# Kernel optimization log

Hardware: AMD Instinct MI355X
Metric: run time of the kernel (lower is better)

## Reference

```python
import jax, jax.numpy as jnp
import numpy as np

H = 16        # num_heads
LN_EPS = 1e-6

def _ln(x, w, b):
    mu = x.mean(-1, keepdims=True)
    var = ((x - mu) ** 2).mean(-1, keepdims=True)
    return (x - mu) * jax.lax.rsqrt(var + LN_EPS) * w + b

def setup_inputs():
    key = jax.random.key(0)
    ks = jax.random.split(key, 6)
    B, L, S, D = 2, 8192, 512, 1024
    std = 0.02
    return {
        "q_in": jax.random.normal(ks[0], (B, L, D), jnp.float32),
        "kv_in": jax.random.normal(ks[1], (B, S, D), jnp.float32),
        "qn_w": jnp.ones((D,), jnp.float32),
        "qn_b": jnp.zeros((D,), jnp.float32),
        "kvn_w": jnp.ones((D,), jnp.float32),
        "kvn_b": jnp.zeros((D,), jnp.float32),
        "Wq": jax.random.normal(ks[2], (D, D), jnp.float32) * std,
        "Wk": jax.random.normal(ks[3], (D, D), jnp.float32) * std,
        "Wv": jax.random.normal(ks[4], (D, D), jnp.float32) * std,
        "Wo": jax.random.normal(ks[5], (D, D), jnp.float32) * std,
        "bo": jnp.zeros((D,), jnp.float32),
        "gate": jnp.ones((1,), jnp.float32),
    }

def reference(q_in, kv_in, qn_w, qn_b, kvn_w, kvn_b, Wq, Wk, Wv, Wo, bo, gate):
    b, l, hid = q_in.shape
    s = kv_in.shape[1]
    d = hid // H
    scale = d ** -0.5
    q_x = _ln(q_in, qn_w, qn_b)
    kv_x = _ln(kv_in, kvn_w, kvn_b)
    # torch Linear: y = x @ W.T  (weights stored [out, in])
    q = (q_x @ Wq.T).reshape(b, l, H, d).transpose(0, 2, 1, 3)   # [b,H,l,d]
    k = (kv_x @ Wk.T).reshape(b, s, H, d).transpose(0, 2, 1, 3)  # [b,H,s,d]
    v = (kv_x @ Wv.T).reshape(b, s, H, d).transpose(0, 2, 1, 3)  # [b,H,s,d]
    logits = jnp.einsum('bhld,bhsd->bhls', q, k) * scale
    attn = jax.nn.softmax(logits, axis=-1)                       # [b,H,l,s]
    # no-grad diagnostics
    attn_d = jax.lax.stop_gradient(attn).astype(jnp.float32)
    ent_per_head = -(attn_d * jnp.log(attn_d + 1e-9)).sum(-1).mean(axis=(0, 2))  # [H]
    mean_entropy = ent_per_head.mean()
    head_entropy_std = ent_per_head.std()  # population std (unbiased=False)
    top_k = min(4, s)
    top_mass = jax.lax.top_k(attn_d, top_k)[0].sum(-1).mean()
    out = jnp.einsum('bhls,bhsd->bhld', attn, v)
    out = out.transpose(0, 2, 1, 3).reshape(b, l, hid)
    out = (out @ Wo.T + bo) * gate  # dropout=0 -> identity; gate broadcasts
    return (out, mean_entropy, head_entropy_std, top_mass, gate[0])
```

## Files before the change

kernel.cpp:

```cpp
#include <hip/hip_runtime.h>
#include <stdint.h>
#include <stddef.h>


typedef __attribute__((ext_vector_type(8))) short bf16x8;
typedef __attribute__((ext_vector_type(4))) float f32x4;

#define MFMA(a, b, c) __builtin_amdgcn_mfma_f32_16x16x32_bf16((a), (b), (c), 0, 0, 0)
#define MED3(a, b, c) __builtin_amdgcn_fmed3f((a), (b), (c))

__device__ __forceinline__ float bf2f(unsigned short u) {
  union { unsigned int ui; float f; } cv; cv.ui = ((unsigned int)u) << 16; return cv.f;
}
__device__ __forceinline__ unsigned short f2bf(float f) {
  union { float f; unsigned int ui; } cv; cv.f = f;
  unsigned int u = cv.ui;
  u = u + 0x7fffu + ((u >> 16) & 1u);
  return (unsigned short)(u >> 16);
}
__device__ __forceinline__ unsigned int pk2(float a, float b) {
  union { float f; unsigned int u; } ua, ub; ua.f = a; ub.f = b;
  return __builtin_amdgcn_perm(ub.u, ua.u, 0x07060302u);
}
__device__ __forceinline__ bool is_fp32(const unsigned int* probe) {
  return probe[0] == 0x3F800000u;
}
__device__ __forceinline__ void gl2lds(const unsigned short* g, unsigned short* l) {
  __builtin_amdgcn_global_load_lds(
      (const __attribute__((address_space(1))) void*)(uintptr_t)g,
      (__attribute__((address_space(3))) void*)(unsigned int)(uintptr_t)l,
      16, 0, 0);
}

__device__ __forceinline__ size_t qf_addr(int qg, int d) {
  int b = qg >> 13, q = qg & 8191, h = d >> 6, dd = d & 63;
  int lane = (q & 15) | (((dd >> 3) & 3) << 4);
  return ((((size_t)(b * 16 + h) * 512 + (q >> 4)) * 2 + (dd >> 5)) * 64 + lane) * 8 + (dd & 7);
}
__device__ __forceinline__ size_t kf_addr(int r, int d) {
  int b = r >> 9, s = r & 511, h = d >> 6, dd = d & 63;
  int lane = (s & 15) | (((dd >> 3) & 3) << 4);
  return ((((size_t)(b * 16 + h) * 32 + (s >> 4)) * 2 + (dd >> 5)) * 64 + lane) * 8 + (dd & 7);
}
__device__ __forceinline__ size_t vf_addr(int r, int d) {
  int b = r >> 9, s = r & 511, h = d >> 6, dd = d & 63;
  int lane = (dd & 15) | (((s >> 3) & 3) << 4);
  return ((((size_t)(b * 16 + h) * 16 + (s >> 5)) * 4 + (dd >> 4)) * 64 + lane) * 8 + (s & 7);
}

__device__ __forceinline__ void ln_row_impl(
    bool f32, const void* __restrict__ xv, const void* __restrict__ wv,
    const void* __restrict__ bv, unsigned short* __restrict__ y,
    int row, int tid, float* rs, float* rs2)
{
  float v0, v1, v2, v3, w0, w1, w2, w3, b0, b1, b2, b3;
  if (f32) {
    float4 xr = *(const float4*)((const float*)xv + (size_t)row * 1024 + tid * 4);
    v0 = xr.x; v1 = xr.y; v2 = xr.z; v3 = xr.w;
    float4 wr = *(const float4*)((const float*)wv + tid * 4);
    w0 = wr.x; w1 = wr.y; w2 = wr.z; w3 = wr.w;
    float4 br = *(const float4*)((const float*)bv + tid * 4);
    b0 = br.x; b1 = br.y; b2 = br.z; b3 = br.w;
  } else {
    ushort4 xr = *(const ushort4*)((const unsigned short*)xv + (size_t)row * 1024 + tid * 4);
    v0 = bf2f(xr.x); v1 = bf2f(xr.y); v2 = bf2f(xr.z); v3 = bf2f(xr.w);
    ushort4 wr = *(const ushort4*)((const unsigned short*)wv + tid * 4);
    w0 = bf2f(wr.x); w1 = bf2f(wr.y); w2 = bf2f(wr.z); w3 = bf2f(wr.w);
    ushort4 br = *(const ushort4*)((const unsigned short*)bv + tid * 4);
    b0 = bf2f(br.x); b1 = bf2f(br.y); b2 = bf2f(br.z); b3 = bf2f(br.w);
  }
  float s  = v0 + v1 + v2 + v3;
  float s2 = v0*v0 + v1*v1 + v2*v2 + v3*v3;
  #pragma unroll
  for (int off = 32; off > 0; off >>= 1) {
    s  += __shfl_xor(s, off);
    s2 += __shfl_xor(s2, off);
  }
  if ((tid & 63) == 0) { rs[tid >> 6] = s; rs2[tid >> 6] = s2; }
  __syncthreads();
  s  = rs[0] + rs[1] + rs[2] + rs[3];
  s2 = rs2[0] + rs2[1] + rs2[2] + rs2[3];
  const float mean = s * (1.0f / 1024.0f);
  const float var  = s2 * (1.0f / 1024.0f) - mean * mean;
  const float rstd = 1.0f / sqrtf(var + 1e-6f);
  ushort4 o;
  o.x = f2bf((v0 - mean) * rstd * w0 + b0);
  o.y = f2bf((v1 - mean) * rstd * w1 + b1);
  o.z = f2bf((v2 - mean) * rstd * w2 + b2);
  o.w = f2bf((v3 - mean) * rstd * w3 + b3);
  *(ushort4*)(y + (size_t)row * 1024 + tid * 4) = o;
}

__global__ __launch_bounds__(256) void ln_q_kernel(
    const unsigned int* __restrict__ probe,
    const void* __restrict__ xv, const void* __restrict__ wv,
    const void* __restrict__ bv, unsigned short* __restrict__ y)
{
  __shared__ float rs[4], rs2[4];
  ln_row_impl(is_fp32(probe), xv, wv, bv, y, blockIdx.x, threadIdx.x, rs, rs2);
}

__global__ __launch_bounds__(256) void prep_all(
    const unsigned int* __restrict__ probe,
    const void* __restrict__ w0, const void* __restrict__ w1,
    const void* __restrict__ w2, const void* __restrict__ w3,
    unsigned short* __restrict__ wdst,
    const void* __restrict__ kv_in, const void* __restrict__ kvn_w,
    const void* __restrict__ kvn_b, unsigned short* __restrict__ kvx,
    const void* __restrict__ bo, const void* __restrict__ gate,
    unsigned short* __restrict__ bob, unsigned short* __restrict__ gateb,
    float* __restrict__ stats)
{
  __shared__ float rs[4], rs2[4];
  const bool f32 = is_fp32(probe);
  const int bx = blockIdx.x, tid = threadIdx.x;
  if (bx < 4096) {
    const int m = bx >> 10;
    const void* src = (m == 0) ? w0 : (m == 1) ? w1 : (m == 2) ? w2 : w3;
    unsigned short* d = wdst + (size_t)m * 1048576;
    const int i = (bx & 1023) * 1024 + tid * 4;
    ushort4 o;
    if (f32) {
      float4 v = *(const float4*)((const float*)src + i);
      o.x = f2bf(v.x); o.y = f2bf(v.y); o.z = f2bf(v.z); o.w = f2bf(v.w);
    } else {
      o = *(const ushort4*)((const unsigned short*)src + i);
    }
    *(ushort4*)(d + i) = o;
  } else if (bx < 5120) {
    ln_row_impl(f32, kv_in, kvn_w, kvn_b, kvx, bx - 4096, tid, rs, rs2);
  } else {
    ushort4 o;
    if (f32) {
      float4 v = *(const float4*)((const float*)bo + tid * 4);
      o.x = f2bf(v.x); o.y = f2bf(v.y); o.z = f2bf(v.z); o.w = f2bf(v.w);
    } else {
      o = *(const ushort4*)((const unsigned short*)bo + tid * 4);
    }
    *(ushort4*)(bob + tid * 4) = o;
    if (tid == 0)
      gateb[0] = f32 ? f2bf(((const float*)gate)[0]) : ((const unsigned short*)gate)[0];
    if (tid < 17) stats[tid] = 0.0f;
  }
}

template <int MODE>
__global__ __launch_bounds__(256, 3) void gemm_nt(
    const unsigned int* __restrict__ probe,
    const unsigned short* __restrict__ A, const unsigned short* __restrict__ B,
    void* __restrict__ Cv, int M, int N, int K,
    const unsigned short* __restrict__ bias, const unsigned short* __restrict__ gate)
{
  __shared__ unsigned short As[128 * 64];
  __shared__ unsigned short Bs[128 * 64];
  const int tid = threadIdx.x;
  const int n0 = blockIdx.x * 128, m0 = blockIdx.y * 128;
  const int wave = tid >> 6, lane = tid & 63, ln = lane & 15, quad = lane >> 4;
  const int wm = (wave >> 1) * 64, wn = (wave & 1) * 64;
  f32x4 acc[4][4] = {};
  for (int k0 = 0; k0 < K; k0 += 64) {
    __syncthreads();
    #pragma unroll
    for (int i = 0; i < 4; i++) {
      int idx = tid + i * 256;
      int r = idx >> 3, ch = (idx & 7) * 8;
      gl2lds(A + (size_t)(m0 + r) * K + k0 + ch, As + r * 64 + ch);
      gl2lds(B + (size_t)(n0 + r) * K + k0 + ch, Bs + r * 64 + ch);
    }
    __syncthreads();
    #pragma unroll
    for (int kk = 0; kk < 64; kk += 32) {
      bf16x8 af[4], bfr[4];
      #pragma unroll
      for (int i = 0; i < 4; i++) {
        af[i]  = *(const bf16x8*)(As + (wm + i * 16 + ln) * 64 + kk + quad * 8);
        bfr[i] = *(const bf16x8*)(Bs + (wn + i * 16 + ln) * 64 + kk + quad * 8);
      }
      #pragma unroll
      for (int mi = 0; mi < 4; mi++)
        #pragma unroll
        for (int ni = 0; ni < 4; ni++)
          acc[mi][ni] = MFMA(af[mi], bfr[ni], acc[mi][ni]);
    }
  }
  const bool f32o = (MODE == 1) && is_fp32(probe);
  const float g = (MODE == 1) ? bf2f(gate[0]) : 1.0f;
  #pragma unroll
  for (int mi = 0; mi < 4; mi++) {
    #pragma unroll
    for (int ni = 0; ni < 4; ni++) {
      const int col = n0 + wn + ni * 16 + ln;
      const float badd = (MODE == 1) ? bf2f(bias[col]) : 0.0f;
      #pragma unroll
      for (int r = 0; r < 4; r++) {
        const int row = m0 + wm + mi * 16 + quad * 4 + r;
        const float val = (acc[mi][ni][r] + badd) * g;
        if (MODE == 1) {
          if (f32o) ((float*)Cv)[(size_t)row * N + col] = val;
          else ((unsigned short*)Cv)[(size_t)row * N + col] = f2bf(val);
        } else if (MODE == 2) {
          ((unsigned short*)Cv)[qf_addr(row, col)] = f2bf(val * 0.18033688f);
        } else {
          if (col < 1024) ((unsigned short*)Cv)[kf_addr(row, col)] = f2bf(val);
          else ((unsigned short*)Cv)[1048576 + vf_addr(row, col - 1024)] = f2bf(val);
        }
      }
    }
  }
}

#define PPAD 40
__global__ __launch_bounds__(256, 3) void attn_kernel(
    const unsigned short* __restrict__ Qf, const unsigned short* __restrict__ Kf,
    const unsigned short* __restrict__ Vf, unsigned short* __restrict__ ctx,
    float* __restrict__ stats)
{
  __shared__ unsigned short Pt[4 * 32 * PPAD];
  __shared__ float red_e[4], red_t[4];
  const int tid = threadIdx.x;
  const int wave = tid >> 6, lane = tid & 63, ln = lane & 15, quad = lane >> 4;
  const int qc = blockIdx.x & 63;
  const int bh = blockIdx.x >> 6;
  const int h = bh & 15, bb = bh >> 4;
  const int qt0 = qc * 8 + wave * 2;

  const unsigned short* qfb = Qf + (((size_t)bh * 512 + qt0) * 2 * 64 + lane) * 8;
  bf16x8 bq00 = *(const bf16x8*)(qfb);
  bf16x8 bq01 = *(const bf16x8*)(qfb + 512);
  bf16x8 bq10 = *(const bf16x8*)(qfb + 1024);
  bf16x8 bq11 = *(const bf16x8*)(qfb + 1536);

  const unsigned short* kfb = Kf + ((size_t)bh * 64 * 64 + lane) * 8;
  const unsigned short* vfb = Vf + ((size_t)bh * 64 * 64 + lane) * 8;

  float l0 = 0.f, l1 = 0.f, s10 = 0.f, s11 = 0.f;
  float ta0 = -1e30f, ta1 = -1e30f, ta2 = -1e30f, ta3 = -1e30f;
  float tb0 = -1e30f, tb1 = -1e30f, tb2 = -1e30f, tb3 = -1e30f;
  f32x4 O0[4] = {}, O1[4] = {};
  unsigned short* Pw = Pt + wave * 32 * PPAD;

  for (int ch = 0; ch < 16; ch++) {
    const unsigned short* kp = kfb + (size_t)ch * 2048;
    const unsigned short* vp = vfb + (size_t)ch * 2048;
    bf16x8 ka0 = *(const bf16x8*)(kp);
    bf16x8 ka1 = *(const bf16x8*)(kp + 512);
    bf16x8 kb0 = *(const bf16x8*)(kp + 1024);
    bf16x8 kb1 = *(const bf16x8*)(kp + 1536);
    bf16x8 vf0 = *(const bf16x8*)(vp);
    bf16x8 vf1 = *(const bf16x8*)(vp + 512);
    bf16x8 vf2 = *(const bf16x8*)(vp + 1024);
    bf16x8 vf3 = *(const bf16x8*)(vp + 1536);

    f32x4 a00 = {}, a01 = {}, a10 = {}, a11 = {};
    a00 = MFMA(ka0, bq00, a00); a00 = MFMA(ka1, bq01, a00);
    a01 = MFMA(ka0, bq10, a01); a01 = MFMA(ka1, bq11, a01);
    a10 = MFMA(kb0, bq00, a10); a10 = MFMA(kb1, bq01, a10);
    a11 = MFMA(kb0, bq10, a11); a11 = MFMA(kb1, bq11, a11);

    #pragma unroll
    for (int r = 0; r < 4; r++) {
      {
        float x = a00[r];
        float o0 = ta0, o1 = ta1, o2 = ta2;
        ta0 = fmaxf(o0, x); ta1 = MED3(o0, o1, x); ta2 = MED3(o1, o2, x); ta3 = MED3(o2, ta3, x);
        float p = exp2f(x); l0 += p; s10 = fmaf(p, x, s10); a00[r] = p;
      }
      {
        float x = a10[r];
        float o0 = ta0, o1 = ta1, o2 = ta2;
        ta0 = fmaxf(o0, x); ta1 = MED3(o0, o1, x); ta2 = MED3(o1, o2, x); ta3 = MED3(o2, ta3, x);
        float p = exp2f(x); l0 += p; s10 = fmaf(p, x, s10); a10[r] = p;
      }
      {
        float x = a01[r];
        float o0 = tb0, o1 = tb1, o2 = tb2;
        tb0 = fmaxf(o0, x); tb1 = MED3(o0, o1, x); tb2 = MED3(o1, o2, x); tb3 = MED3(o2, tb3, x);
        float p = exp2f(x); l1 += p; s11 = fmaf(p, x, s11); a01[r] = p;
      }
      {
        float x = a11[r];
        float o0 = tb0, o1 = tb1, o2 = tb2;
        tb0 = fmaxf(o0, x); tb1 = MED3(o0, o1, x); tb2 = MED3(o1, o2, x); tb3 = MED3(o2, tb3, x);
        float p = exp2f(x); l1 += p; s11 = fmaf(p, x, s11); a11[r] = p;
      }
    }

    {
      uint2 w;
      w.x = pk2(a00[0], a00[1]); w.y = pk2(a00[2], a00[3]);
      *(uint2*)(Pw + (ln) * PPAD + quad * 4) = w;
      w.x = pk2(a10[0], a10[1]); w.y = pk2(a10[2], a10[3]);
      *(uint2*)(Pw + (ln) * PPAD + 16 + quad * 4) = w;
      w.x = pk2(a01[0], a01[1]); w.y = pk2(a01[2], a01[3]);
      *(uint2*)(Pw + (16 + ln) * PPAD + quad * 4) = w;
      w.x = pk2(a11[0], a11[1]); w.y = pk2(a11[2], a11[3]);
      *(uint2*)(Pw + (16 + ln) * PPAD + 16 + quad * 4) = w;
    }
    const bf16x8 pa0 = *(const bf16x8*)(Pw + ln * PPAD + quad * 8);
    const bf16x8 pa1 = *(const bf16x8*)(Pw + (16 + ln) * PPAD + quad * 8);

    O0[0] = MFMA(pa0, vf0, O0[0]); O0[1] = MFMA(pa0, vf1, O0[1]);
    O0[2] = MFMA(pa0, vf2, O0[2]); O0[3] = MFMA(pa0, vf3, O0[3]);
    O1[0] = MFMA(pa1, vf0, O1[0]); O1[1] = MFMA(pa1, vf1, O1[1]);
    O1[2] = MFMA(pa1, vf2, O1[2]); O1[3] = MFMA(pa1, vf3, O1[3]);
  }

  float esum = 0.f, tsum = 0.f, invl0, invl1;
  #pragma unroll
  for (int qi = 0; qi < 2; qi++) {
    float lq = qi ? l1 : l0, sq = qi ? s11 : s10;
    float a0 = qi ? tb0 : ta0, a1 = qi ? tb1 : ta1, a2 = qi ? tb2 : ta2, a3 = qi ? tb3 : ta3;
    lq += __shfl_xor(lq, 16); lq += __shfl_xor(lq, 32);
    sq += __shfl_xor(sq, 16); sq += __shfl_xor(sq, 32);
    #pragma unroll
    for (int off = 16; off <= 32; off <<= 1) {
      float o0 = __shfl_xor(a0, off), o1 = __shfl_xor(a1, off);
      float o2 = __shfl_xor(a2, off), o3 = __shfl_xor(a3, off);
      float c0 = fmaxf(a0, o3), c1 = fmaxf(a1, o2), c2 = fmaxf(a2, o1), c3 = fmaxf(a3, o0);
      float d0 = fmaxf(c0, c2), d2v = fminf(c0, c2), d1 = fmaxf(c1, c3), d3v = fminf(c1, c3);
      a0 = fmaxf(d0, d1); a1 = fminf(d0, d1); a2 = fmaxf(d2v, d3v); a3 = fminf(d2v, d3v);
    }
    const float invl = 1.0f / lq;
    esum += 0.69314718f * (__log2f(lq) - sq * invl);
    tsum += (exp2f(a0) + exp2f(a1) + exp2f(a2) + exp2f(a3)) * invl;
    if (qi) invl1 = invl; else invl0 = invl;
  }
  #pragma unroll
  for (int off = 1; off < 64; off <<= 1) {
    esum += __shfl_xor(esum, off);
    tsum += __shfl_xor(tsum, off);
  }
  if (lane == 0) { red_e[wave] = esum * 0.25f; red_t[wave] = tsum * 0.25f; }
  __syncthreads();
  if (tid == 0) {
    atomicAdd(&stats[h],  red_e[0] + red_e[1] + red_e[2] + red_e[3]);
    atomicAdd(&stats[16], red_t[0] + red_t[1] + red_t[2] + red_t[3]);
  }

  const size_t rb = (size_t)bb * 8192 + (size_t)qt0 * 16 + quad * 4;
  #pragma unroll
  for (int nt = 0; nt < 4; nt++) {
    const int col = h * 64 + nt * 16 + ln;
    #pragma unroll
    for (int r = 0; r < 4; r++) {
      ctx[(rb + r) * 1024 + col]      = f2bf(O0[nt][r] * invl0);
      ctx[(rb + 16 + r) * 1024 + col] = f2bf(O1[nt][r] * invl1);
    }
  }
}

__global__ void finalize_kernel(const unsigned int* __restrict__ probe,
                                const float* __restrict__ stats,
                                const unsigned short* __restrict__ gateb,
                                void* __restrict__ out)
{
  if (threadIdx.x != 0) return;
  const bool f32 = is_fp32(probe);
  float e[16], s = 0.0f;
  for (int i = 0; i < 16; i++) { e[i] = stats[i] * (1.0f / 16384.0f); s += e[i]; }
  const float mean = s * (1.0f / 16.0f);
  float var = 0.0f;
  for (int i = 0; i < 16; i++) { float d = e[i] - mean; var += d * d; }
  var *= (1.0f / 16.0f);
  const float stdv = sqrtf(var);
  const float tm = stats[16] * (1.0f / 262144.0f);
  const float gv = bf2f(gateb[0]);
  if (f32) {
    float* t = (float*)out + 16777216;
    t[0] = mean; t[1] = stdv; t[2] = tm; t[3] = gv;
  } else {
    unsigned short* t = (unsigned short*)out + 16777216;
    t[0] = f2bf(mean); t[1] = f2bf(stdv); t[2] = f2bf(tm); t[3] = f2bf(gv);
  }
}

extern "C" void kernel_launch(void* const* d_in, const int* in_sizes, int n_in,
                              void* d_out, int out_size, void* d_ws, size_t ws_size,
                              hipStream_t stream)
{
  const void* q_in  = d_in[0];
  const void* kv_in = d_in[1];
  const unsigned int* probe = (const unsigned int*)d_in[2];
  const void* qn_w  = d_in[2];
  const void* qn_b  = d_in[3];
  const void* kvn_w = d_in[4];
  const void* kvn_b = d_in[5];
  const void* Wq    = d_in[6];
  const void* Wk    = d_in[7];
  const void* Wv    = d_in[8];
  const void* Wo    = d_in[9];
  const void* bo    = d_in[10];
  const void* gate  = d_in[11];

  unsigned short* ws    = (unsigned short*)d_ws;
  unsigned short* qx    = ws;
  unsigned short* kvx   = qx + 16777216;
  unsigned short* kfrag = kvx + 1048576;
  unsigned short* vfrag = kfrag + 1048576;
  unsigned short* wcv   = vfrag + 1048576;
  unsigned short* bob   = wcv + 4194304;
  unsigned short* gateb = bob + 1024;
  float* stats = (float*)(gateb + 8);
  unsigned short* qfrag = (unsigned short*)d_out;

  prep_all<<<5121, 256, 0, stream>>>(probe, Wq, Wk, Wv, Wo, wcv,
                                     kv_in, kvn_w, kvn_b, kvx,
                                     bo, gate, bob, gateb, stats);
  ln_q_kernel<<<16384, 256, 0, stream>>>(probe, q_in, qn_w, qn_b, qx);
  gemm_nt<2><<<dim3(8, 128), 256, 0, stream>>>(probe, qx, wcv, qfrag,
                                               16384, 1024, 1024, nullptr, nullptr);
  gemm_nt<5><<<dim3(16, 8), 256, 0, stream>>>(probe, kvx, wcv + 1048576, kfrag,
                                              1024, 2048, 1024, nullptr, nullptr);
  attn_kernel<<<2048, 256, 0, stream>>>(qfrag, kfrag, vfrag, qx , stats);
  gemm_nt<1><<<dim3(8, 128), 256, 0, stream>>>(probe, qx, wcv + 3145728, d_out,
                                               16384, 1024, 1024, bob, gateb);
  finalize_kernel<<<1, 64, 0, stream>>>(probe, stats, gateb, d_out);
}
```

Baseline: 377.7 us.

## Fuse launches, swizzle GEMM tiles per XCD, prefetch K and split softmax accumulators

The q LayerNorm moves into the prep kernel, and the Q and KV projection GEMMs merge into one launch whose tiles are mapped per XCD. The output GEMM also gets an XCD-aware tile swizzle. In attention, K fragments for the next chunk are prefetched, MFMA blocks are wrapped in s_setprio, the row-sum, entropy and top-4 accumulators are split into two independent chains merged at the end, and exp2f is replaced by the hardware v_exp_f32. The aim is to cut launch overhead, improve L2 locality and shorten dependency chains in the softmax loop. Risks are a small accuracy difference from the raw exp instruction and an extra K load past the last chunk.

```diff
diff --git a/kernel.cpp b/kernel.cpp
--- a/kernel.cpp
+++ b/kernel.cpp
@@ -21,6 +21,13 @@
 __device__ __forceinline__ unsigned int pk2(float a, float b) {
   union { float f; unsigned int u; } ua, ub; ua.f = a; ub.f = b;
   return __builtin_amdgcn_perm(ub.u, ua.u, 0x07060302u);
+}
+__device__ __forceinline__ float ex2(float x) {
+#if __has_builtin(__builtin_amdgcn_exp2f)
+  return __builtin_amdgcn_exp2f(x);
+#else
+  float r; asm("v_exp_f32 %0, %1" : "=v"(r) : "v"(x)); return r;
+#endif
 }
 __device__ __forceinline__ bool is_fp32(const unsigned int* probe) {
   return probe[0] == 0x3F800000u;
@@ -91,17 +98,10 @@
   *(ushort4*)(y + (size_t)row * 1024 + tid * 4) = o;
 }
 
-__global__ __launch_bounds__(256) void ln_q_kernel(
-    const unsigned int* __restrict__ probe,
-    const void* __restrict__ xv, const void* __restrict__ wv,
-    const void* __restrict__ bv, unsigned short* __restrict__ y)
-{
-  __shared__ float rs[4], rs2[4];
-  ln_row_impl(is_fp32(probe), xv, wv, bv, y, blockIdx.x, threadIdx.x, rs, rs2);
-}
-
 __global__ __launch_bounds__(256) void prep_all(
     const unsigned int* __restrict__ probe,
+    const void* __restrict__ q_in, const void* __restrict__ qn_w,
+    const void* __restrict__ qn_b, unsigned short* __restrict__ qx,
     const void* __restrict__ w0, const void* __restrict__ w1,
     const void* __restrict__ w2, const void* __restrict__ w3,
     unsigned short* __restrict__ wdst,
@@ -114,11 +114,16 @@
   __shared__ float rs[4], rs2[4];
   const bool f32 = is_fp32(probe);
   const int bx = blockIdx.x, tid = threadIdx.x;
-  if (bx < 4096) {
-    const int m = bx >> 10;
+  if (bx < 16384) {
+    ln_row_impl(f32, q_in, qn_w, qn_b, qx, bx, tid, rs, rs2);
+    return;
+  }
+  const int b2 = bx - 16384;
+  if (b2 < 4096) {
+    const int m = b2 >> 10;
     const void* src = (m == 0) ? w0 : (m == 1) ? w1 : (m == 2) ? w2 : w3;
     unsigned short* d = wdst + (size_t)m * 1048576;
-    const int i = (bx & 1023) * 1024 + tid * 4;
+    const int i = (b2 & 1023) * 1024 + tid * 4;
     ushort4 o;
     if (f32) {
       float4 v = *(const float4*)((const float*)src + i);
@@ -127,8 +132,8 @@
       o = *(const ushort4*)((const unsigned short*)src + i);
     }
     *(ushort4*)(d + i) = o;
-  } else if (bx < 5120) {
-    ln_row_impl(f32, kv_in, kvn_w, kvn_b, kvx, bx - 4096, tid, rs, rs2);
+  } else if (b2 < 5120) {
+    ln_row_impl(f32, kv_in, kvn_w, kvn_b, kvx, b2 - 4096, tid, rs, rs2);
   } else {
     ushort4 o;
     if (f32) {
@@ -145,16 +150,14 @@
 }
 
 template <int MODE>
-__global__ __launch_bounds__(256, 3) void gemm_nt(
+__device__ __forceinline__ void gemm_core(
     const unsigned int* __restrict__ probe,
     const unsigned short* __restrict__ A, const unsigned short* __restrict__ B,
-    void* __restrict__ Cv, int M, int N, int K,
-    const unsigned short* __restrict__ bias, const unsigned short* __restrict__ gate)
-{
-  __shared__ unsigned short As[128 * 64];
-  __shared__ unsigned short Bs[128 * 64];
+    void* __restrict__ Cv, int N, int K, int m0, int n0,
+    const unsigned short* __restrict__ bias, const unsigned short* __restrict__ gate,
+    unsigned short* As, unsigned short* Bs)
+{
   const int tid = threadIdx.x;
-  const int n0 = blockIdx.x * 128, m0 = blockIdx.y * 128;
   const int wave = tid >> 6, lane = tid & 63, ln = lane & 15, quad = lane >> 4;
   const int wm = (wave >> 1) * 64, wn = (wave & 1) * 64;
   f32x4 acc[4][4] = {};
@@ -209,6 +212,46 @@
   }
 }
 
+template <int MODE>
+__global__ __launch_bounds__(256, 3) void gemm_nt(
+    const unsigned int* __restrict__ probe,
+    const unsigned short* __restrict__ A, const unsigned short* __restrict__ B,
+    void* __restrict__ Cv, int M, int N, int K,
+    const unsigned short* __restrict__ bias, const unsigned short* __restrict__ gate)
+{
+  __shared__ unsigned short As[128 * 64];
+  __shared__ unsigned short Bs[128 * 64];
+  const int nbx = gridDim.x;
+  const int nwg = nbx * gridDim.y;
+  const int cpx = nwg >> 3;
+  const int flat = blockIdx.y * nbx + blockIdx.x;
+  const int swz = (flat & 7) * cpx + (flat >> 3);
+  const int n0 = (swz % nbx) * 128;
+  const int m0 = (swz / nbx) * 128;
+  gemm_core<MODE>(probe, A, B, Cv, N, K, m0, n0, bias, gate, As, Bs);
+}
+
+__global__ __launch_bounds__(256, 3) void gemm_qkv(
+    const unsigned int* __restrict__ probe,
+    const unsigned short* __restrict__ qx, const unsigned short* __restrict__ kvx,
+    const unsigned short* __restrict__ wcv,
+    unsigned short* __restrict__ qfrag, unsigned short* __restrict__ kvfrag)
+{
+  __shared__ unsigned short As[128 * 64];
+  __shared__ unsigned short Bs[128 * 64];
+  const int flat = blockIdx.x;
+  const int xcd = flat & 7, local = flat >> 3;
+  if (local < 16) {
+    const int id = xcd * 16 + local;
+    gemm_core<5>(probe, kvx, wcv + 1048576, kvfrag, 2048, 1024,
+                 (id >> 4) * 128, (id & 15) * 128, nullptr, nullptr, As, Bs);
+  } else {
+    const int id = xcd * 128 + (local - 16);
+    gemm_core<2>(probe, qx, wcv, qfrag, 1024, 1024,
+                 (id >> 3) * 128, (id & 7) * 128, nullptr, nullptr, As, Bs);
+  }
+}
+
 #define PPAD 40
 __global__ __launch_bounds__(256, 3) void attn_kernel(
     const unsigned short* __restrict__ Qf, const unsigned short* __restrict__ Kf,
@@ -233,29 +276,42 @@
   const unsigned short* kfb = Kf + ((size_t)bh * 64 * 64 + lane) * 8;
   const unsigned short* vfb = Vf + ((size_t)bh * 64 * 64 + lane) * 8;
 
-  float l0 = 0.f, l1 = 0.f, s10 = 0.f, s11 = 0.f;
+  float l0a = 0.f, l0b = 0.f, l1a = 0.f, l1b = 0.f;
+  float s0a = 0.f, s0b = 0.f, s1a = 0.f, s1b = 0.f;
   float ta0 = -1e30f, ta1 = -1e30f, ta2 = -1e30f, ta3 = -1e30f;
   float tb0 = -1e30f, tb1 = -1e30f, tb2 = -1e30f, tb3 = -1e30f;
+  float tc0 = -1e30f, tc1 = -1e30f, tc2 = -1e30f, tc3 = -1e30f;
+  float td0 = -1e30f, td1 = -1e30f, td2 = -1e30f, td3 = -1e30f;
   f32x4 O0[4] = {}, O1[4] = {};
   unsigned short* Pw = Pt + wave * 32 * PPAD;
 
+  bf16x8 ka0 = *(const bf16x8*)(kfb);
+  bf16x8 ka1 = *(const bf16x8*)(kfb + 512);
+  bf16x8 kb0 = *(const bf16x8*)(kfb + 1024);
+  bf16x8 kb1 = *(const bf16x8*)(kfb + 1536);
+
   for (int ch = 0; ch < 16; ch++) {
-    const unsigned short* kp = kfb + (size_t)ch * 2048;
     const unsigned short* vp = vfb + (size_t)ch * 2048;
-    bf16x8 ka0 = *(const bf16x8*)(kp);
-    bf16x8 ka1 = *(const bf16x8*)(kp + 512);
-    bf16x8 kb0 = *(const bf16x8*)(kp + 1024);
-    bf16x8 kb1 = *(const bf16x8*)(kp + 1536);
     bf16x8 vf0 = *(const bf16x8*)(vp);
     bf16x8 vf1 = *(const bf16x8*)(vp + 512);
     bf16x8 vf2 = *(const bf16x8*)(vp + 1024);
     bf16x8 vf3 = *(const bf16x8*)(vp + 1536);
 
     f32x4 a00 = {}, a01 = {}, a10 = {}, a11 = {};
+    __builtin_amdgcn_s_setprio(1);
     a00 = MFMA(ka0, bq00, a00); a00 = MFMA(ka1, bq01, a00);
     a01 = MFMA(ka0, bq10, a01); a01 = MFMA(ka1, bq11, a01);
     a10 = MFMA(kb0, bq00, a10); a10 = MFMA(kb1, bq01, a10);
     a11 = MFMA(kb0, bq10, a11); a11 = MFMA(kb1, bq11, a11);
+    __builtin_amdgcn_s_setprio(0);
+
+    {
+      const unsigned short* kp = kfb + (size_t)(ch + 1) * 2048;
+      ka0 = *(const bf16x8*)(kp);
+      ka1 = *(const bf16x8*)(kp + 512);
+      kb0 = *(const bf16x8*)(kp + 1024);
+      kb1 = *(const bf16x8*)(kp + 1536);
+    }
 
     #pragma unroll
     for (int r = 0; r < 4; r++) {
@@ -263,25 +319,25 @@
         float x = a00[r];
         float o0 = ta0, o1 = ta1, o2 = ta2;
         ta0 = fmaxf(o0, x); ta1 = MED3(o0, o1, x); ta2 = MED3(o1, o2, x); ta3 = MED3(o2, ta3, x);
-        float p = exp2f(x); l0 += p; s10 = fmaf(p, x, s10); a00[r] = p;
+        float p = ex2(x); l0a += p; s0a = fmaf(p, x, s0a); a00[r] = p;
       }
       {
         float x = a10[r];
-        float o0 = ta0, o1 = ta1, o2 = ta2;
-        ta0 = fmaxf(o0, x); ta1 = MED3(o0, o1, x); ta2 = MED3(o1, o2, x); ta3 = MED3(o2, ta3, x);
-        float p = exp2f(x); l0 += p; s10 = fmaf(p, x, s10); a10[r] = p;
+        float o0 = tc0, o1 = tc1, o2 = tc2;
+        tc0 = fmaxf(o0, x); tc1 = MED3(o0, o1, x); tc2 = MED3(o1, o2, x); tc3 = MED3(o2, tc3, x);
+        float p = ex2(x); l0b += p; s0b = fmaf(p, x, s0b); a10[r] = p;
       }
       {
         float x = a01[r];
         float o0 = tb0, o1 = tb1, o2 = tb2;
         tb0 = fmaxf(o0, x); tb1 = MED3(o0, o1, x); tb2 = MED3(o1, o2, x); tb3 = MED3(o2, tb3, x);
-        float p = exp2f(x); l1 += p; s11 = fmaf(p, x, s11); a01[r] = p;
+        float p = ex2(x); l1a += p; s1a = fmaf(p, x, s1a); a01[r] = p;
       }
       {
         float x = a11[r];
-        float o0 = tb0, o1 = tb1, o2 = tb2;
-        tb0 = fmaxf(o0, x); tb1 = MED3(o0, o1, x); tb2 = MED3(o1, o2, x); tb3 = MED3(o2, tb3, x);
-        float p = exp2f(x); l1 += p; s11 = fmaf(p, x, s11); a11[r] = p;
+        float o0 = td0, o1 = td1, o2 = td2;
+        td0 = fmaxf(o0, x); td1 = MED3(o0, o1, x); td2 = MED3(o1, o2, x); td3 = MED3(o2, td3, x);
+        float p = ex2(x); l1b += p; s1b = fmaf(p, x, s1b); a11[r] = p;
       }
     }
 
@@ -299,10 +355,25 @@
     const bf16x8 pa0 = *(const bf16x8*)(Pw + ln * PPAD + quad * 8);
     const bf16x8 pa1 = *(const bf16x8*)(Pw + (16 + ln) * PPAD + quad * 8);
 
+    __builtin_amdgcn_s_setprio(1);
     O0[0] = MFMA(pa0, vf0, O0[0]); O0[1] = MFMA(pa0, vf1, O0[1]);
     O0[2] = MFMA(pa0, vf2, O0[2]); O0[3] = MFMA(pa0, vf3, O0[3]);
     O1[0] = MFMA(pa1, vf0, O1[0]); O1[1] = MFMA(pa1, vf1, O1[1]);
     O1[2] = MFMA(pa1, vf2, O1[2]); O1[3] = MFMA(pa1, vf3, O1[3]);
+    __builtin_amdgcn_s_setprio(0);
+  }
+
+  float l0 = l0a + l0b, l1 = l1a + l1b;
+  float s10 = s0a + s0b, s11 = s1a + s1b;
+  {
+    float c0 = fmaxf(ta0, tc3), c1 = fmaxf(ta1, tc2), c2 = fmaxf(ta2, tc1), c3 = fmaxf(ta3, tc0);
+    float d0 = fmaxf(c0, c2), d2v = fminf(c0, c2), d1 = fmaxf(c1, c3), d3v = fminf(c1, c3);
+    ta0 = fmaxf(d0, d1); ta1 = fminf(d0, d1); ta2 = fmaxf(d2v, d3v); ta3 = fminf(d2v, d3v);
+  }
+  {
+    float c0 = fmaxf(tb0, td3), c1 = fmaxf(tb1, td2), c2 = fmaxf(tb2, td1), c3 = fmaxf(tb3, td0);
+    float d0 = fmaxf(c0, c2), d2v = fminf(c0, c2), d1 = fmaxf(c1, c3), d3v = fminf(c1, c3);
+    tb0 = fmaxf(d0, d1); tb1 = fminf(d0, d1); tb2 = fmaxf(d2v, d3v); tb3 = fminf(d2v, d3v);
   }
 
   float esum = 0.f, tsum = 0.f, invl0, invl1;
@@ -322,7 +393,7 @@
     }
     const float invl = 1.0f / lq;
     esum += 0.69314718f * (__log2f(lq) - sq * invl);
-    tsum += (exp2f(a0) + exp2f(a1) + exp2f(a2) + exp2f(a3)) * invl;
+    tsum += (ex2(a0) + ex2(a1) + ex2(a2) + ex2(a3)) * invl;
     if (qi) invl1 = invl; else invl0 = invl;
   }
   #pragma unroll
@@ -403,14 +474,11 @@
   float* stats = (float*)(gateb + 8);
   unsigned short* qfrag = (unsigned short*)d_out;
 
-  prep_all<<<5121, 256, 0, stream>>>(probe, Wq, Wk, Wv, Wo, wcv,
-                                     kv_in, kvn_w, kvn_b, kvx,
-                                     bo, gate, bob, gateb, stats);
-  ln_q_kernel<<<16384, 256, 0, stream>>>(probe, q_in, qn_w, qn_b, qx);
-  gemm_nt<2><<<dim3(8, 128), 256, 0, stream>>>(probe, qx, wcv, qfrag,
-                                               16384, 1024, 1024, nullptr, nullptr);
-  gemm_nt<5><<<dim3(16, 8), 256, 0, stream>>>(probe, kvx, wcv + 1048576, kfrag,
-                                              1024, 2048, 1024, nullptr, nullptr);
+  prep_all<<<21505, 256, 0, stream>>>(probe, q_in, qn_w, qn_b, qx,
+                                      Wq, Wk, Wv, Wo, wcv,
+                                      kv_in, kvn_w, kvn_b, kvx,
+                                      bo, gate, bob, gateb, stats);
+  gemm_qkv<<<1152, 256, 0, stream>>>(probe, qx, kvx, wcv, qfrag, kfrag);
   attn_kernel<<<2048, 256, 0, stream>>>(qfrag, kfrag, vfrag, qx , stats);
   gemm_nt<1><<<dim3(8, 128), 256, 0, stream>>>(probe, qx, wcv + 3145728, d_out,
                                                16384, 1024, 1024, bob, gateb);
```

After: 319.4 us. -15.4%, faster.
